# Kernel optimization log

Measured on AMD Instinct MI355X. Metric: run time of the kernel, lower is better.

Reference implementation:

```python
import jax, jax.numpy as jnp
import numpy as np

EPI_AGE_PENALTY = 0.02
EPI_MIN_STRENGTH = 0.001
EPI_STRENGTH_BOOST = 0.5
RMS_EPS = 1e-6


def setup_inputs() -> dict:
    key = jax.random.key(0)
    k1, k2, k3, k4, k5, k6 = jax.random.split(key, 6)
    B, S, D = 32, 8192, 512
    return {
        "q_win": jax.random.normal(k1, (B, D), dtype=jnp.float32),
        "epi_keys": jax.random.normal(k2, (B, S, D), dtype=jnp.float32),
        "epi_vals": jax.random.normal(k3, (B, S, D), dtype=jnp.float32),
        "epi_age": jax.random.uniform(k4, (B, S), dtype=jnp.float32),
        "epi_strength": jax.random.uniform(k5, (B, S), dtype=jnp.float32),
        "scale": jnp.ones((D,), dtype=jnp.float32),  # RMSNorm learned scale
    }


def reference(q_win, epi_keys, epi_vals, epi_age, epi_strength, scale):
    # L2-normalize query [B,D] and keys [B,S,D]
    qn = q_win / (jnp.linalg.norm(q_win, axis=-1, keepdims=True) + 1e-6)
    kn = epi_keys / (jnp.linalg.norm(epi_keys, axis=-1, keepdims=True) + 1e-6)
    # cosine similarity [B,S]
    sim = jnp.einsum("bsd,bd->bs", kn, qn)
    str_log = jnp.log(jnp.clip(epi_strength, EPI_MIN_STRENGTH, 1e9))
    logits = sim + EPI_STRENGTH_BOOST * str_log - EPI_AGE_PENALTY * epi_age
    alive = (epi_strength > EPI_MIN_STRENGTH).astype(jnp.float32)
    logits = logits + (alive - 1.0) * 1000.0
    w = jax.nn.softmax(logits, axis=-1)
    # softmax-weighted read over slots -> [B,D]
    read = jnp.einsum("bs,bsd->bd", w, epi_vals)
    # RMSNorm
    rms = jnp.sqrt(jnp.mean(jnp.square(read), axis=-1, keepdims=True) + RMS_EPS)
    read = read / rms * scale
    return (read, w, logits)
```

## Files before the change

### kernel.cpp

```cpp
#include <hip/hip_runtime.h>
#include <math.h>

#define BB 32
#define SS 8192
#define DD 512
#define D4 (DD / 4)
#define CHUNKS 64
#define CHUNK 128

static constexpr float AGE_PEN = 0.02f;
static constexpr float MIN_STR = 0.001f;
static constexpr float STR_BOOST = 0.5f;
static constexpr float RMS_EPS_F = 1e-6f;

__device__ inline float dot4(float4 a, float4 b) {
    return a.x * b.x + a.y * b.y + a.z * b.z + a.w * b.w;
}

__device__ inline float block_sum(float v, volatile float* red) {
    int tid = threadIdx.x, lane = tid & 63, wid = tid >> 6;
#pragma unroll
    for (int off = 32; off; off >>= 1) v += __shfl_xor(v, off);
    if (lane == 0) red[wid] = v;
    __syncthreads();
    float r = red[0] + red[1] + red[2] + red[3];
    __syncthreads();
    return r;
}

__global__ __launch_bounds__(256) void logits_e_kernel(
    const float4* __restrict__ keys, const float* __restrict__ q,
    const float* __restrict__ age, const float* __restrict__ strength,
    float* __restrict__ logits, float* __restrict__ e_out) {
    int wid = threadIdx.x >> 6, lane = threadIdx.x & 63;
    int row = blockIdx.x * 4 + wid;
    int b = row >> 13;

    const float4* q4 = (const float4*)q + b * D4;
    float4 q0 = q4[lane], q1 = q4[lane + 64];
    float qq = dot4(q0, q0) + dot4(q1, q1);
#pragma unroll
    for (int off = 32; off; off >>= 1) qq += __shfl_xor(qq, off);
    float qinv = 1.f / (sqrtf(qq) + 1e-6f);

    const float4* k = keys + (long long)row * D4;
    float4 k0 = k[lane], k1 = k[lane + 64];
    float kk = dot4(k0, k0) + dot4(k1, k1);
    float kq = dot4(k0, q0) + dot4(k1, q1);
#pragma unroll
    for (int off = 32; off; off >>= 1) {
        kk += __shfl_xor(kk, off);
        kq += __shfl_xor(kq, off);
    }
    if (lane == 0) {
        float st = strength[row];
        float a = age[row];
        float sim = kq * qinv / (sqrtf(kk) + 1e-6f);
        float lg = sim + STR_BOOST * logf(fminf(fmaxf(st, MIN_STR), 1e9f)) - AGE_PEN * a;
        if (!(st > MIN_STR)) lg -= 1000.f;
        logits[row] = lg;
        e_out[row] = expf(lg);
    }
}

__global__ __launch_bounds__(128) void wsum_kernel(
    const float4* __restrict__ vals, const float* __restrict__ e,
    float4* __restrict__ partial, float* __restrict__ esum_partial) {
    __shared__ float sw[CHUNK];
    __shared__ float rede[2];
    int chunk = blockIdx.x, b = blockIdx.y, tid = threadIdx.x;
    int s0 = chunk * CHUNK;
    float my_e = e[b * SS + s0 + tid];
    sw[tid] = my_e;
    __syncthreads();

    const float4* vbase = vals + ((long long)b * SS + s0) * D4 + tid;
    float4 acc = {0.f, 0.f, 0.f, 0.f};
#pragma unroll 4
    for (int s = 0; s < CHUNK; s++) {
        float4 v = vbase[(long long)s * D4];
        float ww = sw[s];
        acc.x += ww * v.x;
        acc.y += ww * v.y;
        acc.z += ww * v.z;
        acc.w += ww * v.w;
    }
    partial[((long long)b * CHUNKS + chunk) * D4 + tid] = acc;

    float t = my_e;
#pragma unroll
    for (int off = 32; off; off >>= 1) t += __shfl_xor(t, off);
    if ((tid & 63) == 0) rede[tid >> 6] = t;
    __syncthreads();
    if (tid == 0) esum_partial[b * CHUNKS + chunk] = rede[0] + rede[1];
}

__global__ __launch_bounds__(256) void reduce_rms_kernel(
    const float* __restrict__ partial, const float* __restrict__ esum_partial,
    const float* __restrict__ scale, float* __restrict__ readout,
    float* __restrict__ inv_esum) {
    __shared__ float red[4];
    int b = blockIdx.x, tid = threadIdx.x;

    const float* p = partial + (long long)b * CHUNKS * DD;
    float r0 = 0.f, r1 = 0.f;
#pragma unroll 4
    for (int c = 0; c < CHUNKS; c++) {
        r0 += p[c * DD + tid];
        r1 += p[c * DD + tid + 256];
    }
    float le = (tid < CHUNKS) ? esum_partial[b * CHUNKS + tid] : 0.f;
    float etot = block_sum(le, red);
    float inv_e = 1.f / etot;
    if (tid == 0) inv_esum[b] = inv_e;
    r0 *= inv_e;
    r1 *= inv_e;
    float ss = block_sum(r0 * r0 + r1 * r1, red);
    float rms = sqrtf(ss / (float)DD + RMS_EPS_F);
    float inv = 1.f / rms;
    readout[b * DD + tid] = r0 * inv * scale[tid];
    readout[b * DD + tid + 256] = r1 * inv * scale[tid + 256];
}

__global__ __launch_bounds__(256) void w_scale_kernel(float4* __restrict__ w,
                                                      const float* __restrict__ inv_esum) {
    int i4 = blockIdx.x * 256 + threadIdx.x;
    int b = i4 >> 11;
    float inv = inv_esum[b];
    float4 v = w[i4];
    v.x *= inv; v.y *= inv; v.z *= inv; v.w *= inv;
    w[i4] = v;
}

extern "C" void kernel_launch(void* const* d_in, const int* in_sizes, int n_in,
                              void* d_out, int out_size, void* d_ws, size_t ws_size,
                              hipStream_t stream) {
    const float* q        = (const float*)d_in[0];
    const float* keys     = (const float*)d_in[1];
    const float* vals     = (const float*)d_in[2];
    const float* age      = (const float*)d_in[3];
    const float* strength = (const float*)d_in[4];
    const float* scale    = (const float*)d_in[5];

    float* out = (float*)d_out;
    float* readout = out;
    float* w       = out + BB * DD;
    float* logits  = out + BB * DD + BB * SS;

    float* ws = (float*)d_ws;
    float* partial      = ws;
    float* esum_partial = ws + BB * CHUNKS * DD;
    float* inv_esum     = esum_partial + BB * CHUNKS;

    logits_e_kernel<<<BB * SS / 4, 256, 0, stream>>>(
        (const float4*)keys, q, age, strength, logits, w);
    wsum_kernel<<<dim3(CHUNKS, BB), 128, 0, stream>>>(
        (const float4*)vals, w, (float4*)partial, esum_partial);
    reduce_rms_kernel<<<BB, 256, 0, stream>>>(partial, esum_partial, scale, readout, inv_esum);
    w_scale_kernel<<<BB * SS / 4 / 256, 256, 0, stream>>>((float4*)w, inv_esum);
}
```

Before: 201.7 us.

## Process four rows per wave, use nontemporal loads, split wsum slots across two groups

The logits kernel now has each wavefront handle four consecutive key rows. It issues eight nontemporal vector loads up front and batches the shuffle reductions, so more memory requests are in flight and the query normalisation is recomputed less often. The weighted-sum kernel doubles its block to 256 threads, with two groups covering the even and odd slots of each chunk and combining their partial sums through shared memory. Both kernels stream their 512 MB inputs with nontemporal hints to limit cache pollution. The trade-offs are higher register pressure and an extra shared-memory reduction step.

```diff
diff --git a/kernel.cpp b/kernel.cpp
--- a/kernel.cpp
+++ b/kernel.cpp
@@ -13,7 +13,9 @@
 static constexpr float STR_BOOST = 0.5f;
 static constexpr float RMS_EPS_F = 1e-6f;
 
-__device__ inline float dot4(float4 a, float4 b) {
+typedef float vf4 __attribute__((ext_vector_type(4)));
+
+__device__ inline float dot4v(vf4 a, vf4 b) {
     return a.x * b.x + a.y * b.y + a.z * b.z + a.w * b.w;
 }
 
@@ -29,70 +31,107 @@
 }
 
 __global__ __launch_bounds__(256) void logits_e_kernel(
-    const float4* __restrict__ keys, const float* __restrict__ q,
-    const float* __restrict__ age, const float* __restrict__ strength,
-    float* __restrict__ logits, float* __restrict__ e_out) {
+    const vf4* __restrict__ keys, const vf4* __restrict__ q,
+    const vf4* __restrict__ age, const vf4* __restrict__ strength,
+    vf4* __restrict__ logits4, vf4* __restrict__ e4) {
     int wid = threadIdx.x >> 6, lane = threadIdx.x & 63;
-    int row = blockIdx.x * 4 + wid;
-    int b = row >> 13;
+    int quad = blockIdx.x * 4 + wid;
+    int row0 = quad * 4;
+    int b = row0 >> 13;
 
-    const float4* q4 = (const float4*)q + b * D4;
-    float4 q0 = q4[lane], q1 = q4[lane + 64];
-    float qq = dot4(q0, q0) + dot4(q1, q1);
+    const vf4* qp = q + b * D4;
+    vf4 q0 = qp[lane], q1 = qp[lane + 64];
+    float qq = dot4v(q0, q0) + dot4v(q1, q1);
 #pragma unroll
     for (int off = 32; off; off >>= 1) qq += __shfl_xor(qq, off);
     float qinv = 1.f / (sqrtf(qq) + 1e-6f);
 
-    const float4* k = keys + (long long)row * D4;
-    float4 k0 = k[lane], k1 = k[lane + 64];
-    float kk = dot4(k0, k0) + dot4(k1, k1);
-    float kq = dot4(k0, q0) + dot4(k1, q1);
+    const vf4* k = keys + (long long)row0 * D4;
+    vf4 ka0 = __builtin_nontemporal_load(k + lane);
+    vf4 ka1 = __builtin_nontemporal_load(k + lane + 64);
+    vf4 kb0 = __builtin_nontemporal_load(k + lane + 128);
+    vf4 kb1 = __builtin_nontemporal_load(k + lane + 192);
+    vf4 kc0 = __builtin_nontemporal_load(k + lane + 256);
+    vf4 kc1 = __builtin_nontemporal_load(k + lane + 320);
+    vf4 kd0 = __builtin_nontemporal_load(k + lane + 384);
+    vf4 kd1 = __builtin_nontemporal_load(k + lane + 448);
+
+    float kk0 = dot4v(ka0, ka0) + dot4v(ka1, ka1);
+    float kq0 = dot4v(ka0, q0) + dot4v(ka1, q1);
+    float kk1 = dot4v(kb0, kb0) + dot4v(kb1, kb1);
+    float kq1 = dot4v(kb0, q0) + dot4v(kb1, q1);
+    float kk2 = dot4v(kc0, kc0) + dot4v(kc1, kc1);
+    float kq2 = dot4v(kc0, q0) + dot4v(kc1, q1);
+    float kk3 = dot4v(kd0, kd0) + dot4v(kd1, kd1);
+    float kq3 = dot4v(kd0, q0) + dot4v(kd1, q1);
+
 #pragma unroll
     for (int off = 32; off; off >>= 1) {
-        kk += __shfl_xor(kk, off);
-        kq += __shfl_xor(kq, off);
+        kk0 += __shfl_xor(kk0, off); kq0 += __shfl_xor(kq0, off);
+        kk1 += __shfl_xor(kk1, off); kq1 += __shfl_xor(kq1, off);
+        kk2 += __shfl_xor(kk2, off); kq2 += __shfl_xor(kq2, off);
+        kk3 += __shfl_xor(kk3, off); kq3 += __shfl_xor(kq3, off);
     }
+
+    vf4 stv = strength[quad];
+    vf4 agv = age[quad];
+
+    float lg0 = kq0 * qinv / (sqrtf(kk0) + 1e-6f)
+              + STR_BOOST * logf(fminf(fmaxf(stv.x, MIN_STR), 1e9f)) - AGE_PEN * agv.x;
+    if (!(stv.x > MIN_STR)) lg0 -= 1000.f;
+    float lg1 = kq1 * qinv / (sqrtf(kk1) + 1e-6f)
+              + STR_BOOST * logf(fminf(fmaxf(stv.y, MIN_STR), 1e9f)) - AGE_PEN * agv.y;
+    if (!(stv.y > MIN_STR)) lg1 -= 1000.f;
+    float lg2 = kq2 * qinv / (sqrtf(kk2) + 1e-6f)
+              + STR_BOOST * logf(fminf(fmaxf(stv.z, MIN_STR), 1e9f)) - AGE_PEN * agv.z;
+    if (!(stv.z > MIN_STR)) lg2 -= 1000.f;
+    float lg3 = kq3 * qinv / (sqrtf(kk3) + 1e-6f)
+              + STR_BOOST * logf(fminf(fmaxf(stv.w, MIN_STR), 1e9f)) - AGE_PEN * agv.w;
+    if (!(stv.w > MIN_STR)) lg3 -= 1000.f;
+
     if (lane == 0) {
-        float st = strength[row];
-        float a = age[row];
-        float sim = kq * qinv / (sqrtf(kk) + 1e-6f);
-        float lg = sim + STR_BOOST * logf(fminf(fmaxf(st, MIN_STR), 1e9f)) - AGE_PEN * a;
-        if (!(st > MIN_STR)) lg -= 1000.f;
-        logits[row] = lg;
-        e_out[row] = expf(lg);
+        vf4 lgv; lgv.x = lg0; lgv.y = lg1; lgv.z = lg2; lgv.w = lg3;
+        logits4[quad] = lgv;
+        vf4 ev; ev.x = expf(lg0); ev.y = expf(lg1); ev.z = expf(lg2); ev.w = expf(lg3);
+        e4[quad] = ev;
     }
 }
 
-__global__ __launch_bounds__(128) void wsum_kernel(
-    const float4* __restrict__ vals, const float* __restrict__ e,
-    float4* __restrict__ partial, float* __restrict__ esum_partial) {
+__global__ __launch_bounds__(256) void wsum_kernel(
+    const vf4* __restrict__ vals, const float* __restrict__ e,
+    vf4* __restrict__ partial, float* __restrict__ esum_partial) {
     __shared__ float sw[CHUNK];
+    __shared__ vf4 racc[D4];
     __shared__ float rede[2];
     int chunk = blockIdx.x, b = blockIdx.y, tid = threadIdx.x;
+    int c = tid & 127, g = tid >> 7;
     int s0 = chunk * CHUNK;
-    float my_e = e[b * SS + s0 + tid];
-    sw[tid] = my_e;
-    __syncthreads();
 
-    const float4* vbase = vals + ((long long)b * SS + s0) * D4 + tid;
-    float4 acc = {0.f, 0.f, 0.f, 0.f};
-#pragma unroll 4
-    for (int s = 0; s < CHUNK; s++) {
-        float4 v = vbase[(long long)s * D4];
-        float ww = sw[s];
-        acc.x += ww * v.x;
-        acc.y += ww * v.y;
-        acc.z += ww * v.z;
-        acc.w += ww * v.w;
+    if (tid < CHUNK) {
+        float my_e = e[b * SS + s0 + tid];
+        sw[tid] = my_e;
+        float t = my_e;
+#pragma unroll
+        for (int off = 32; off; off >>= 1) t += __shfl_xor(t, off);
+        if ((tid & 63) == 0) rede[tid >> 6] = t;
     }
-    partial[((long long)b * CHUNKS + chunk) * D4 + tid] = acc;
-
-    float t = my_e;
-#pragma unroll
-    for (int off = 32; off; off >>= 1) t += __shfl_xor(t, off);
-    if ((tid & 63) == 0) rede[tid >> 6] = t;
     __syncthreads();
     if (tid == 0) esum_partial[b * CHUNKS + chunk] = rede[0] + rede[1];
+
+    const vf4* vbase = vals + ((long long)b * SS + s0) * D4 + c;
+    vf4 acc = {0.f, 0.f, 0.f, 0.f};
+#pragma unroll 8
+    for (int i = 0; i < CHUNK / 2; i++) {
+        int s = 2 * i + g;
+        vf4 v = __builtin_nontemporal_load(vbase + (long long)s * D4);
+        acc += sw[s] * v;
+    }
+    if (g == 1) racc[c] = acc;
+    __syncthreads();
+    if (g == 0) {
+        vf4 o = racc[c] + acc;
+        partial[((long long)b * CHUNKS + chunk) * D4 + c] = o;
+    }
 }
 
 __global__ __launch_bounds__(256) void reduce_rms_kernel(
@@ -122,14 +161,12 @@
     readout[b * DD + tid + 256] = r1 * inv * scale[tid + 256];
 }
 
-__global__ __launch_bounds__(256) void w_scale_kernel(float4* __restrict__ w,
+__global__ __launch_bounds__(256) void w_scale_kernel(vf4* __restrict__ w,
                                                       const float* __restrict__ inv_esum) {
     int i4 = blockIdx.x * 256 + threadIdx.x;
     int b = i4 >> 11;
     float inv = inv_esum[b];
-    float4 v = w[i4];
-    v.x *= inv; v.y *= inv; v.z *= inv; v.w *= inv;
-    w[i4] = v;
+    w[i4] = w[i4] * inv;
 }
 
 extern "C" void kernel_launch(void* const* d_in, const int* in_sizes, int n_in,
@@ -152,10 +189,11 @@
     float* esum_partial = ws + BB * CHUNKS * DD;
     float* inv_esum     = esum_partial + BB * CHUNKS;
 
-    logits_e_kernel<<<BB * SS / 4, 256, 0, stream>>>(
-        (const float4*)keys, q, age, strength, logits, w);
-    wsum_kernel<<<dim3(CHUNKS, BB), 128, 0, stream>>>(
-        (const float4*)vals, w, (float4*)partial, esum_partial);
+    logits_e_kernel<<<BB * SS / 16, 256, 0, stream>>>(
+        (const vf4*)keys, (const vf4*)q, (const vf4*)age, (const vf4*)strength,
+        (vf4*)logits, (vf4*)w);
+    wsum_kernel<<<dim3(CHUNKS, BB), 256, 0, stream>>>(
+        (const vf4*)vals, w, (vf4*)partial, esum_partial);
     reduce_rms_kernel<<<BB, 256, 0, stream>>>(partial, esum_partial, scale, readout, inv_esum);
-    w_scale_kernel<<<BB * SS / 4 / 256, 256, 0, stream>>>((float4*)w, inv_esum);
+    w_scale_kernel<<<BB * SS / 4 / 256, 256, 0, stream>>>((vf4*)w, inv_esum);
 }
```

New measurement: 176.7 us. 1.14x faster.
